# Optimization experiments

Hardware: AMD Instinct MI355X
Metric: run time of the kernel (lower is better)

Reference implementation:

```python
import jax, jax.numpy as jnp
import numpy as np
from jax import lax

B, L, I, H, O = 4096, 60, 13, 128, 2  # batch, seq len (fixed by Linear), input, hidden, output


def _lstm_dir(x, w_ih, w_hh, b_ih, b_hh, reverse):
    """Single-direction LSTM, PyTorch gate order (i, f, g, o). x: [B, L, In] -> [B, L, H]."""
    Hn = w_hh.shape[1]
    # Precompute input projection for all timesteps: [L, B, 4H]
    xp = jnp.einsum('bli,gi->lbg', x, w_ih) + b_ih + b_hh

    def step(carry, xt):
        h, c = carry
        gates = xt + h @ w_hh.T
        i, f, g, o = jnp.split(gates, 4, axis=-1)
        c = jax.nn.sigmoid(f) * c + jax.nn.sigmoid(i) * jnp.tanh(g)
        h = jax.nn.sigmoid(o) * jnp.tanh(c)
        return (h, c), h

    init = (jnp.zeros((x.shape[0], Hn), x.dtype), jnp.zeros((x.shape[0], Hn), x.dtype))
    _, hs = lax.scan(step, init, xp, reverse=reverse)  # outputs kept in original time order
    return jnp.swapaxes(hs, 0, 1)


def _bilstm(x, wf, hf, bif, bhf, wb, hb, bib, bhb):
    fwd = _lstm_dir(x, wf, hf, bif, bhf, False)
    bwd = _lstm_dir(x, wb, hb, bib, bhb, True)
    return jnp.concatenate([fwd, bwd], axis=-1)  # [B, L, 2H]


def setup_inputs() -> dict:
    key = jax.random.key(0)
    ks = iter(jax.random.split(key, 40))

    def p(shape, s=0.08):
        return jax.random.normal(next(ks), shape, dtype=jnp.float32) * s

    d = {"x": jax.random.normal(next(ks), (B, L, I), dtype=jnp.float32)}
    ins = [I, 2 * H, 2 * H]
    for l in range(3):
        for suf in ("f", "b"):
            d[f"w_ih_{l}{suf}"] = p((4 * H, ins[l]))
            d[f"w_hh_{l}{suf}"] = p((4 * H, H))
            d[f"b_ih_{l}{suf}"] = p((4 * H,))
            d[f"b_hh_{l}{suf}"] = p((4 * H,))
    d["w_out"] = p((O, 2 * H * L))
    d["b_out"] = p((O,))
    return d


def reference(x,
              w_ih_0f, w_hh_0f, b_ih_0f, b_hh_0f, w_ih_0b, w_hh_0b, b_ih_0b, b_hh_0b,
              w_ih_1f, w_hh_1f, b_ih_1f, b_hh_1f, w_ih_1b, w_hh_1b, b_ih_1b, b_hh_1b,
              w_ih_2f, w_hh_2f, b_ih_2f, b_hh_2f, w_ih_2b, w_hh_2b, b_ih_2b, b_hh_2b,
              w_out, b_out):
    y = _bilstm(x, w_ih_0f, w_hh_0f, b_ih_0f, b_hh_0f, w_ih_0b, w_hh_0b, b_ih_0b, b_hh_0b)
    y = _bilstm(y, w_ih_1f, w_hh_1f, b_ih_1f, b_hh_1f, w_ih_1b, w_hh_1b, b_ih_1b, b_hh_1b)
    y = _bilstm(y, w_ih_2f, w_hh_2f, b_ih_2f, b_hh_2f, w_ih_2b, w_hh_2b, b_ih_2b, b_hh_2b)
    y = jax.nn.relu(y.reshape(y.shape[0], -1))  # [B, 2H*L]
    return y @ w_out.T + b_out  # [B, O]
```

## Files before the change

### kernel.cpp

```cpp
#include <hip/hip_runtime.h>
#include <math.h>

#define B_  4096
#define L_  60
#define I_  13
#define H_  128
#define AHP 136

typedef _Float16 half8 __attribute__((ext_vector_type(8)));
typedef _Float16 half4v __attribute__((ext_vector_type(4)));
typedef float float4v __attribute__((ext_vector_type(4)));

__global__ void pack_kernel(const float* __restrict__ src, _Float16* __restrict__ dst,
                            int Ksrc, int n,
                            const float* __restrict__ bih, const float* __restrict__ bhh,
                            float* __restrict__ bias_out) {
    int g0 = blockIdx.x * blockDim.x + threadIdx.x;
    for (int e = g0; e < n; e += gridDim.x * blockDim.x) {
        int j  = e & 7;
        int l  = (e >> 3) & 63;
        int ct = (e >> 9) & 7;
        int w4 = (e >> 12) & 3;
        int kt = e >> 14;
        int nn = (ct >> 1) * 128 + w4 * 32 + (ct & 1) * 16 + (l & 15);
        int k  = kt * 32 + ((l >> 4) << 3) + j;
        dst[e] = (k < Ksrc) ? (_Float16)src[nn * Ksrc + k] : (_Float16)0.f;
    }
    if (bias_out && g0 < 512) bias_out[g0] = bih[g0] + bhh[g0];
}

__device__ __forceinline__ float sigm(float x) {
    return __builtin_amdgcn_rcpf(1.f + __expf(-x));
}
__device__ __forceinline__ float tanh_f(float x) {
    return 1.f - 2.f * __builtin_amdgcn_rcpf(__expf(2.f * x) + 1.f);
}

#define SMEM_HALFS 78080

template <int XT, int IS_L0>
__global__ __launch_bounds__(512)
void lstm_mfma(const float* __restrict__ x0, const _Float16* __restrict__ yin,
               const _Float16* __restrict__ px_f, const _Float16* __restrict__ ph_f,
               const _Float16* __restrict__ px_b, const _Float16* __restrict__ ph_b,
               const float* __restrict__ bias_f, const float* __restrict__ bias_b,
               _Float16* __restrict__ yout)
{
    __shared__ _Float16 sm[SMEM_HALFS];
    _Float16* WH = sm;

    const int tid  = threadIdx.x;
    const int lane = tid & 63;
    const int w    = tid >> 6;
    const int w4   = w & 3;
    const int u    = w >> 2;
    const int dir  = blockIdx.x & 1;
    const int rb   = (blockIdx.x >> 1) * 32;
    const int m    = lane & 15;
    const int q    = lane >> 4;
    const int jc   = w4 * 32 + u * 16 + m;

    const _Float16* __restrict__ px   = dir ? px_b : px_f;
    const _Float16* __restrict__ ph   = dir ? ph_b : ph_f;
    const float*    __restrict__ bias = dir ? bias_b : bias_f;
    const _Float16* __restrict__ pWl  = px + w4 * 4096 + u * 512 + lane * 8;
    const _Float16* __restrict__ WHl  = WH + w4 * 4096 + u * 512 + lane * 8;

    {
        const half8* s8 = (const half8*)ph;
        half8* d8 = (half8*)WH;
        for (int i = tid; i < 8192; i += 512) d8[i] = s8[i];
    }

    float bv[4];
#pragma unroll
    for (int tq = 0; tq < 4; ++tq) bv[tq] = bias[tq * 128 + jc];

    if (IS_L0) {
        _Float16* AH0 = sm + 65536;
        _Float16* AH1 = AH0 + 32 * AHP;
        _Float16* AX  = AH1 + 32 * AHP;
        for (int i = tid; i < 2 * 32 * AHP; i += 512) AH0[i] = (_Float16)0.f;

        half8 bX[4];
#pragma unroll
        for (int tq = 0; tq < 4; ++tq) bX[tq] = *(const half8*)(pWl + tq * 1024);

        float cst[2][4];
#pragma unroll
        for (int rt = 0; rt < 2; ++rt)
#pragma unroll
            for (int r = 0; r < 4; ++r) cst[rt][r] = 0.f;

        for (int s = 0; s < L_; ++s) {
            const int t = dir ? (L_ - 1 - s) : s;
            _Float16* __restrict__ Hprev = (s & 1) ? AH0 : AH1;
            _Float16* __restrict__ Hcur  = (s & 1) ? AH1 : AH0;
            _Float16* __restrict__ AXs   = AX + (s & 1) * 1024;

            if (tid < 256) {
                const int e  = tid * 4;
                const int j0 = e & 7;
                const int ln = (e >> 3) & 63;
                const int rt = e >> 9;
                const int row = rt * 16 + (ln & 15);
                const int kb  = ((ln >> 4) << 3) + j0;
                const float* xr = x0 + (size_t)(rb + row) * (L_ * I_) + t * I_;
                half4v tmp;
#pragma unroll
                for (int jj = 0; jj < 4; ++jj) {
                    int k = kb + jj;
                    tmp[jj] = (k < I_) ? (_Float16)xr[k] : (_Float16)0.f;
                }
                ((half4v*)AXs)[tid] = tmp;
            }

            __syncthreads();

            float4v acc[2][4];
#pragma unroll
            for (int rt = 0; rt < 2; ++rt)
#pragma unroll
                for (int tq = 0; tq < 4; ++tq) {
                    float b = bv[tq];
                    acc[rt][tq] = (float4v){b, b, b, b};
                }

            {
                half8 a0 = *(const half8*)(AXs + lane * 8);
                half8 a1 = *(const half8*)(AXs + 512 + lane * 8);
#pragma unroll
                for (int tq = 0; tq < 4; ++tq) {
                    acc[0][tq] = __builtin_amdgcn_mfma_f32_16x16x32_f16(a0, bX[tq], acc[0][tq], 0, 0, 0);
                    acc[1][tq] = __builtin_amdgcn_mfma_f32_16x16x32_f16(a1, bX[tq], acc[1][tq], 0, 0, 0);
                }
            }

#pragma unroll
            for (int kh = 0; kh < 4; ++kh) {
                half8 a0 = *(const half8*)(Hprev + m * AHP + kh * 32 + q * 8);
                half8 a1 = *(const half8*)(Hprev + (16 + m) * AHP + kh * 32 + q * 8);
#pragma unroll
                for (int tq = 0; tq < 4; ++tq) {
                    half8 b = *(const half8*)(WHl + kh * 16384 + tq * 1024);
                    acc[0][tq] = __builtin_amdgcn_mfma_f32_16x16x32_f16(a0, b, acc[0][tq], 0, 0, 0);
                    acc[1][tq] = __builtin_amdgcn_mfma_f32_16x16x32_f16(a1, b, acc[1][tq], 0, 0, 0);
                }
            }

#pragma unroll
            for (int rt = 0; rt < 2; ++rt)
#pragma unroll
                for (int r = 0; r < 4; ++r) {
                    const float gi = acc[rt][0][r];
                    const float gf = acc[rt][1][r];
                    const float gg = acc[rt][2][r];
                    const float go = acc[rt][3][r];
                    const float cc = sigm(gf) * cst[rt][r] + sigm(gi) * tanh_f(gg);
                    cst[rt][r] = cc;
                    const float hh = sigm(go) * tanh_f(cc);
                    const int row = rt * 16 + q * 4 + r;
                    Hcur[row * AHP + jc] = (_Float16)hh;
                    yout[(size_t)(rb + row) * 15360 + t * 256 + dir * H_ + jc] = (_Float16)hh;
                }
        }
        return;
    }

    _Float16* AH = sm + 65536;
    _Float16* XS = AH + 32 * AHP;
    for (int i = tid; i < 32 * AHP; i += 512) AH[i] = (_Float16)0.f;

    const int c0 = tid * 2;
    const int f0 = c0 >> 6,       l0 = c0 & 63;
    const int f1 = (c0 + 1) >> 6, l1 = (c0 + 1) & 63;
    const _Float16* __restrict__ sb0 =
        yin + (size_t)(rb + (f0 & 1) * 16 + (l0 & 15)) * 15360 + (f0 >> 1) * 32 + (l0 >> 4) * 8;
    const _Float16* __restrict__ sb1 =
        yin + (size_t)(rb + (f1 & 1) * 16 + (l1 & 15)) * 15360 + (f1 >> 1) * 32 + (l1 >> 4) * 8;
    _Float16* __restrict__ xw = XS + c0 * 8;

    {
        const int t0 = dir ? (L_ - 1) : 0;
        *(half8*)xw       = *(const half8*)(sb0 + t0 * 256);
        *(half8*)(xw + 8) = *(const half8*)(sb1 + t0 * 256);
    }

    float cst[2][4];
#pragma unroll
    for (int rt = 0; rt < 2; ++rt)
#pragma unroll
        for (int r = 0; r < 4; ++r) cst[rt][r] = 0.f;

    __syncthreads();

    for (int s = 0; s < L_; ++s) {
        const int t  = dir ? (L_ - 1 - s) : s;
        const int sn = (s + 1 < L_) ? s + 1 : s;
        const int tn = dir ? (L_ - 1 - sn) : sn;

        half8 sg0 = *(const half8*)(sb0 + tn * 256);
        half8 sg1 = *(const half8*)(sb1 + tn * 256);

        half8 bC[4], bN[4];
#pragma unroll
        for (int tq = 0; tq < 4; ++tq) bC[tq] = *(const half8*)(pWl + tq * 1024);

        float4v acc[2][4];
#pragma unroll
        for (int rt = 0; rt < 2; ++rt)
#pragma unroll
            for (int tq = 0; tq < 4; ++tq) {
                float b = bv[tq];
                acc[rt][tq] = (float4v){b, b, b, b};
            }

#pragma unroll
        for (int kh = 0; kh < 4; ++kh) {
            half8 a0 = *(const half8*)(AH + m * AHP + kh * 32 + q * 8);
            half8 a1 = *(const half8*)(AH + (16 + m) * AHP + kh * 32 + q * 8);
#pragma unroll
            for (int tq = 0; tq < 4; ++tq) {
                half8 b = *(const half8*)(WHl + kh * 16384 + tq * 1024);
                acc[0][tq] = __builtin_amdgcn_mfma_f32_16x16x32_f16(a0, b, acc[0][tq], 0, 0, 0);
                acc[1][tq] = __builtin_amdgcn_mfma_f32_16x16x32_f16(a1, b, acc[1][tq], 0, 0, 0);
            }
        }

#pragma unroll
        for (int kt = 0; kt < XT; ++kt) {
            if (kt + 1 < XT) {
#pragma unroll
                for (int tq = 0; tq < 4; ++tq)
                    bN[tq] = *(const half8*)(pWl + (kt + 1) * 16384 + tq * 1024);
            }
            half8 a0 = *(const half8*)(XS + (kt * 2 + 0) * 512 + lane * 8);
            half8 a1 = *(const half8*)(XS + (kt * 2 + 1) * 512 + lane * 8);
#pragma unroll
            for (int tq = 0; tq < 4; ++tq) {
                acc[0][tq] = __builtin_amdgcn_mfma_f32_16x16x32_f16(a0, bC[tq], acc[0][tq], 0, 0, 0);
                acc[1][tq] = __builtin_amdgcn_mfma_f32_16x16x32_f16(a1, bC[tq], acc[1][tq], 0, 0, 0);
            }
            if (kt + 1 < XT) {
#pragma unroll
                for (int tq = 0; tq < 4; ++tq) bC[tq] = bN[tq];
            }
        }

        __syncthreads();

        *(half8*)xw       = sg0;
        *(half8*)(xw + 8) = sg1;

#pragma unroll
        for (int rt = 0; rt < 2; ++rt)
#pragma unroll
            for (int r = 0; r < 4; ++r) {
                const float gi = acc[rt][0][r];
                const float gf = acc[rt][1][r];
                const float gg = acc[rt][2][r];
                const float go = acc[rt][3][r];
                const float cc = sigm(gf) * cst[rt][r] + sigm(gi) * tanh_f(gg);
                cst[rt][r] = cc;
                const float hh = sigm(go) * tanh_f(cc);
                const int row = rt * 16 + q * 4 + r;
                AH[row * AHP + jc] = (_Float16)hh;
                yout[(size_t)(rb + row) * 15360 + t * 256 + dir * H_ + jc] = (_Float16)hh;
            }

        __syncthreads();
    }
}

__global__ __launch_bounds__(256)
void final_kernel(const _Float16* __restrict__ y, const float* __restrict__ wout,
                  const float* __restrict__ bout, float* __restrict__ outp, int nrows) {
    const int wid  = (blockIdx.x * blockDim.x + threadIdx.x) >> 6;
    const int lane = threadIdx.x & 63;
    if (wid >= nrows) return;
    const half8*  __restrict__ y8 = (const half8*)(y + (size_t)wid * 15360);
    const float4* __restrict__ w4 = (const float4*)wout;
    float s0 = 0.f, s1 = 0.f;
#pragma unroll 2
    for (int it = 0; it < 30; ++it) {
        const int idx = it * 64 + lane;
        half8 h = y8[idx];
        float v[8];
#pragma unroll
        for (int e = 0; e < 8; ++e) v[e] = fmaxf((float)h[e], 0.f);
        const float4 a0 = w4[idx * 2], a1 = w4[idx * 2 + 1];
        const float4 b0 = w4[3840 + idx * 2], b1 = w4[3840 + idx * 2 + 1];
        s0 += v[0] * a0.x + v[1] * a0.y + v[2] * a0.z + v[3] * a0.w
            + v[4] * a1.x + v[5] * a1.y + v[6] * a1.z + v[7] * a1.w;
        s1 += v[0] * b0.x + v[1] * b0.y + v[2] * b0.z + v[3] * b0.w
            + v[4] * b1.x + v[5] * b1.y + v[6] * b1.z + v[7] * b1.w;
    }
#pragma unroll
    for (int off = 32; off > 0; off >>= 1) {
        s0 += __shfl_down(s0, off);
        s1 += __shfl_down(s1, off);
    }
    if (lane == 0) {
        outp[wid * 2 + 0] = s0 + bout[0];
        outp[wid * 2 + 1] = s1 + bout[1];
    }
}

extern "C" void kernel_launch(void* const* d_in, const int* in_sizes, int n_in,
                              void* d_out, int out_size, void* d_ws, size_t ws_size,
                              hipStream_t stream) {
    const float* x = (const float*)d_in[0];
    auto W = [&](int l, int d, int which) { return (const float*)d_in[1 + l * 8 + d * 4 + which]; };
    const float* w_out = (const float*)d_in[25];
    const float* b_out = (const float*)d_in[26];

    _Float16* wsH = (_Float16*)d_ws;
    const size_t px0f = 0,       ph0f = 16384;
    const size_t px0b = 81920,   ph0b = 98304;
    const size_t px1f = 163840,  ph1f = 294912;
    const size_t px1b = 360448,  ph1b = 491520;
    const size_t px2f = 557056,  ph2f = 688128;
    const size_t px2b = 753664,  ph2b = 884736;
    const size_t packs_end = 950272;
    float* bias = (float*)(wsH + packs_end);
    const size_t head_bytes = packs_end * 2 + 4096 * 4;
    _Float16* y0 = (_Float16*)((char*)d_ws + head_bytes);

    pack_kernel<<<64, 256, 0, stream>>>(W(0,0,0), wsH + px0f, I_,  16384,  W(0,0,2), W(0,0,3), bias + 0);
    pack_kernel<<<256,256, 0, stream>>>(W(0,0,1), wsH + ph0f, H_,  65536,  nullptr, nullptr, nullptr);
    pack_kernel<<<64, 256, 0, stream>>>(W(0,1,0), wsH + px0b, I_,  16384,  W(0,1,2), W(0,1,3), bias + 512);
    pack_kernel<<<256,256, 0, stream>>>(W(0,1,1), wsH + ph0b, H_,  65536,  nullptr, nullptr, nullptr);
    pack_kernel<<<512,256, 0, stream>>>(W(1,0,0), wsH + px1f, 256, 131072, W(1,0,2), W(1,0,3), bias + 1024);
    pack_kernel<<<256,256, 0, stream>>>(W(1,0,1), wsH + ph1f, H_,  65536,  nullptr, nullptr, nullptr);
    pack_kernel<<<512,256, 0, stream>>>(W(1,1,0), wsH + px1b, 256, 131072, W(1,1,2), W(1,1,3), bias + 1536);
    pack_kernel<<<256,256, 0, stream>>>(W(1,1,1), wsH + ph1b, H_,  65536,  nullptr, nullptr, nullptr);
    pack_kernel<<<512,256, 0, stream>>>(W(2,0,0), wsH + px2f, 256, 131072, W(2,0,2), W(2,0,3), bias + 2048);
    pack_kernel<<<256,256, 0, stream>>>(W(2,0,1), wsH + ph2f, H_,  65536,  nullptr, nullptr, nullptr);
    pack_kernel<<<512,256, 0, stream>>>(W(2,1,0), wsH + px2b, 256, 131072, W(2,1,2), W(2,1,3), bias + 2560);
    pack_kernel<<<256,256, 0, stream>>>(W(2,1,1), wsH + ph2b, H_,  65536,  nullptr, nullptr, nullptr);

    const size_t avail_halfs = (ws_size > head_bytes) ? (ws_size - head_bytes) / 2 : 0;
    int chunks = 1;
    while (chunks < 128 && (size_t)2 * (B_ / chunks) * 15360 > avail_halfs) chunks *= 2;
    const int CB = B_ / chunks;

    _Float16* yA = y0;
    _Float16* yB = y0 + (size_t)CB * 15360;

    for (int c = 0; c < chunks; ++c) {
        const float* xc = x + (size_t)c * CB * (L_ * I_);
        float* outc = (float*)d_out + (size_t)c * CB * 2;
        lstm_mfma<1, 1><<<2 * CB / 32, 512, 0, stream>>>(
            xc, nullptr, wsH + px0f, wsH + ph0f, wsH + px0b, wsH + ph0b, bias + 0, bias + 512, yA);
        lstm_mfma<8, 0><<<2 * CB / 32, 512, 0, stream>>>(
            nullptr, yA, wsH + px1f, wsH + ph1f, wsH + px1b, wsH + ph1b, bias + 1024, bias + 1536, yB);
        lstm_mfma<8, 0><<<2 * CB / 32, 512, 0, stream>>>(
            nullptr, yB, wsH + px2f, wsH + ph2f, wsH + px2b, wsH + ph2b, bias + 2048, bias + 2560, yA);
        final_kernel<<<(CB + 3) / 4, 256, 0, stream>>>(yA, w_out, b_out, outc, CB);
    }
}
```

Baseline: 669.0 us.

## Coalesce hidden-state output stores via LDS and interleave recurrent MFMAs with input MFMAs

The per-element scattered fp16 stores of h to global memory are replaced by one 16-byte vector store per thread, which reads the previous step's hidden tile back from LDS at the start of the next step, plus a final store after the loop. In the upper layers, the recurrent h·W_hh MFMAs are also split across the kt loop over input tiles, so they interleave with the input-projection MFMAs and the B-operand prefetches. The aim is fewer, wider global writes and better overlap of MFMA work with loads. The cost is an extra LDS read per step and an added barrier before the final store in layer 0. The interleaving assumes XT equals 8 so that every recurrent k-chunk and gate is covered.

```diff
diff --git a/kernel.cpp b/kernel.cpp
--- a/kernel.cpp
+++ b/kernel.cpp
@@ -60,6 +60,11 @@
     const int q    = lane >> 4;
     const int jc   = w4 * 32 + u * 16 + m;
 
+    const int crow = tid >> 4;
+    const int ccg  = tid & 15;
+    _Float16* __restrict__ ybase =
+        yout + (size_t)(rb + crow) * 15360 + dir * H_ + ccg * 8;
+
     const _Float16* __restrict__ px   = dir ? px_b : px_f;
     const _Float16* __restrict__ ph   = dir ? ph_b : ph_f;
     const float*    __restrict__ bias = dir ? bias_b : bias_f;
@@ -116,6 +121,12 @@
             }
 
             __syncthreads();
+
+            if (s > 0) {
+                const int tp = dir ? (t + 1) : (t - 1);
+                half8 hv = *(const half8*)(Hprev + crow * AHP + ccg * 8);
+                *(half8*)(ybase + tp * 256) = hv;
+            }
 
             float4v acc[2][4];
 #pragma unroll
@@ -161,8 +172,14 @@
                     const float hh = sigm(go) * tanh_f(cc);
                     const int row = rt * 16 + q * 4 + r;
                     Hcur[row * AHP + jc] = (_Float16)hh;
-                    yout[(size_t)(rb + row) * 15360 + t * 256 + dir * H_ + jc] = (_Float16)hh;
-                }
+                }
+        }
+        __syncthreads();
+        {
+            _Float16* __restrict__ Hl = ((L_ - 1) & 1) ? AH1 : AH0;
+            const int tp = dir ? 0 : (L_ - 1);
+            half8 hv = *(const half8*)(Hl + crow * AHP + ccg * 8);
+            *(half8*)(ybase + tp * 256) = hv;
         }
         return;
     }
@@ -206,6 +223,12 @@
 #pragma unroll
         for (int tq = 0; tq < 4; ++tq) bC[tq] = *(const half8*)(pWl + tq * 1024);
 
+        if (s > 0) {
+            const int tp = dir ? (t + 1) : (t - 1);
+            half8 hv = *(const half8*)(AH + crow * AHP + ccg * 8);
+            *(half8*)(ybase + tp * 256) = hv;
+        }
+
         float4v acc[2][4];
 #pragma unroll
         for (int rt = 0; rt < 2; ++rt)
@@ -216,23 +239,23 @@
             }
 
 #pragma unroll
-        for (int kh = 0; kh < 4; ++kh) {
-            half8 a0 = *(const half8*)(AH + m * AHP + kh * 32 + q * 8);
-            half8 a1 = *(const half8*)(AH + (16 + m) * AHP + kh * 32 + q * 8);
-#pragma unroll
-            for (int tq = 0; tq < 4; ++tq) {
-                half8 b = *(const half8*)(WHl + kh * 16384 + tq * 1024);
-                acc[0][tq] = __builtin_amdgcn_mfma_f32_16x16x32_f16(a0, b, acc[0][tq], 0, 0, 0);
-                acc[1][tq] = __builtin_amdgcn_mfma_f32_16x16x32_f16(a1, b, acc[1][tq], 0, 0, 0);
-            }
-        }
-
-#pragma unroll
         for (int kt = 0; kt < XT; ++kt) {
             if (kt + 1 < XT) {
 #pragma unroll
                 for (int tq = 0; tq < 4; ++tq)
                     bN[tq] = *(const half8*)(pWl + (kt + 1) * 16384 + tq * 1024);
+            }
+            {
+                const int kh  = kt >> 1;
+                const int tqb = (kt & 1) * 2;
+                half8 ha0 = *(const half8*)(AH + m * AHP + kh * 32 + q * 8);
+                half8 ha1 = *(const half8*)(AH + (16 + m) * AHP + kh * 32 + q * 8);
+#pragma unroll
+                for (int e = 0; e < 2; ++e) {
+                    half8 hb = *(const half8*)(WHl + kh * 16384 + (tqb + e) * 1024);
+                    acc[0][tqb + e] = __builtin_amdgcn_mfma_f32_16x16x32_f16(ha0, hb, acc[0][tqb + e], 0, 0, 0);
+                    acc[1][tqb + e] = __builtin_amdgcn_mfma_f32_16x16x32_f16(ha1, hb, acc[1][tqb + e], 0, 0, 0);
+                }
             }
             half8 a0 = *(const half8*)(XS + (kt * 2 + 0) * 512 + lane * 8);
             half8 a1 = *(const half8*)(XS + (kt * 2 + 1) * 512 + lane * 8);
@@ -265,10 +288,15 @@
                 const float hh = sigm(go) * tanh_f(cc);
                 const int row = rt * 16 + q * 4 + r;
                 AH[row * AHP + jc] = (_Float16)hh;
-                yout[(size_t)(rb + row) * 15360 + t * 256 + dir * H_ + jc] = (_Float16)hh;
             }
 
         __syncthreads();
+    }
+
+    {
+        const int tp = dir ? 0 : (L_ - 1);
+        half8 hv = *(const half8*)(AH + crow * AHP + ccg * 8);
+        *(half8*)(ybase + tp * 256) = hv;
     }
 }
 
```

After: 650.5 us (median of 2 runs). 1.03x faster.
